# Kernel optimization log

Measured on AMD Instinct MI355X. Metric: run time of the kernel, lower is better.

The kernel has to match this reference:

```python
import jax, jax.numpy as jnp
import numpy as np

N = 50000        # nodes
E = 1_600_000    # edges (avg degree 32)
IN = 8           # in_channels
OUT = 64         # out_channels / hidden
K = 2            # Chebyshev order


def setup_inputs() -> dict:
    key = jax.random.key(0)
    ks = jax.random.split(key, 16)
    w = lambda k, s: (jax.random.normal(k, s, jnp.float32) * 0.05)
    inp = {
        "x": jax.random.normal(ks[0], (N, IN), jnp.float32),
        "H": jax.random.normal(ks[1], (N, OUT), jnp.float32),
        "edge_index": jax.random.randint(ks[2], (2, E), 0, N, dtype=jnp.int64),
    }
    names = [("z_x", IN), ("z_h", OUT), ("r_x", IN), ("r_h", OUT), ("c_x", IN), ("c_h", OUT)]
    for i, (nm, d) in enumerate(names):
        inp["W_" + nm] = w(ks[3 + 2 * i], (K, d, OUT))
        inp["b_" + nm] = w(ks[4 + 2 * i], (OUT,))
    return inp


def _cheb(x, W, b, row, col, norm):
    # PyG-style ChebConv with lambda_max=2: L_hat = -D^{-1/2} A D^{-1/2}
    # Tx0 = x; Tx1 = L_hat x; Tx_k = 2 L_hat Tx_{k-1} - Tx_{k-2}
    out = x @ W[0]
    Tx0 = x
    Tx1 = jax.ops.segment_sum(norm[:, None] * x[col], row, num_segments=N)
    out = out + Tx1 @ W[1]
    for k in range(2, W.shape[0]):
        Tx2 = 2.0 * jax.ops.segment_sum(norm[:, None] * Tx1[col], row, num_segments=N) - Tx0
        out = out + Tx2 @ W[k]
        Tx0, Tx1 = Tx1, Tx2
    return out + b


def reference(x, H, edge_index, W_z_x, b_z_x, W_z_h, b_z_h, W_r_x, b_r_x,
              W_r_h, b_r_h, W_c_x, b_c_x, W_c_h, b_c_h):
    row, col = edge_index[0], edge_index[1]
    deg = jax.ops.segment_sum(jnp.ones((E,), x.dtype), row, num_segments=N)
    dinv = jnp.where(deg > 0, 1.0 / jnp.sqrt(jnp.where(deg > 0, deg, 1.0)), 0.0)
    norm = -dinv[row] * dinv[col]  # sym-normalized, negated adjacency (L - I)

    Z = jax.nn.sigmoid(_cheb(x, W_z_x, b_z_x, row, col, norm)
                       + _cheb(H, W_z_h, b_z_h, row, col, norm))
    R = jax.nn.sigmoid(_cheb(x, W_r_x, b_r_x, row, col, norm)
                       + _cheb(H, W_r_h, b_r_h, row, col, norm))
    C = jnp.tanh(_cheb(x, W_c_x, b_c_x, row, col, norm)
                 + _cheb(R * H, W_c_h, b_c_h, row, col, norm))
    return Z * H + (1.0 - Z) * C
```

## Files before the change

kernel.cpp:

```cpp
#include <hip/hip_runtime.h>
#include <hip/hip_fp16.h>
#include <math.h>

#define IN_CH 8
#define OUT_CH 64
#define NPW 8

__device__ __forceinline__ unsigned short f2h(float f) {
    return __half_as_ushort(__float2half_rn(f));
}
__device__ __forceinline__ float h2f_lo(unsigned v) {
    return __half2float(__ushort_as_half((unsigned short)(v & 0xFFFFu)));
}
__device__ __forceinline__ float h2f_hi(unsigned v) {
    return __half2float(__ushort_as_half((unsigned short)(v >> 16)));
}
__device__ __forceinline__ float sigmoidf(float v) { return 1.0f / (1.0f + expf(-v)); }

__global__ void degP_kernel(const int* __restrict__ row, int* __restrict__ deg,
                            int E, int RPP) {
    int p = blockIdx.x & 7;
    int sub = blockIdx.x >> 3;
    int nsub = gridDim.x >> 3;
    int lo = p * RPP, hi = lo + RPP;
    for (int e = sub * blockDim.x + threadIdx.x; e < E; e += nsub * blockDim.x) {
        int r = row[e];
        if (r >= lo && r < hi) atomicAdd(&deg[r], 1);
    }
}

__global__ void dinv_kernel(const int* __restrict__ deg, float* __restrict__ dinv, int N) {
    int i = blockIdx.x * blockDim.x + threadIdx.x;
    if (i < N) {
        int d = deg[i];
        dinv[i] = (d > 0) ? rsqrtf((float)d) : 0.f;
    }
}

__global__ void scan_kernel(const int* __restrict__ deg, int* __restrict__ rowptr,
                            int* __restrict__ cursor, int N) {
    __shared__ int s_wave[17];
    __shared__ int s_running;
    int tid = threadIdx.x;
    int lane = tid & 63, wid = tid >> 6;
    if (tid == 0) s_running = 0;
    __syncthreads();
    for (int base = 0; base < N; base += 1024) {
        int i = base + tid;
        int v = (i < N) ? deg[i] : 0;
        int incl = v;
#pragma unroll
        for (int off = 1; off < 64; off <<= 1) {
            int t = __shfl_up(incl, off, 64);
            if (lane >= off) incl += t;
        }
        if (lane == 63) s_wave[wid] = incl;
        __syncthreads();
        if (wid == 0) {
            int wv = (lane < 16) ? s_wave[lane] : 0;
            int winc = wv;
#pragma unroll
            for (int off = 1; off < 16; off <<= 1) {
                int t = __shfl_up(winc, off, 64);
                if (lane >= off) winc += t;
            }
            if (lane < 16) s_wave[lane] = winc - wv;
            if (lane == 15) s_wave[16] = winc;
        }
        __syncthreads();
        int run = s_running;
        int excl = run + s_wave[wid] + incl - v;
        if (i < N) { rowptr[i] = excl; cursor[i] = excl; }
        __syncthreads();
        if (tid == 0) s_running = run + s_wave[16];
        __syncthreads();
    }
    if (tid == 0) rowptr[N] = s_running;
}

__global__ void bucketP_kernel(const int* __restrict__ ei, int* __restrict__ cursor,
                               int* __restrict__ col_s, int E, int RPP) {
    int p = blockIdx.x & 7;
    int sub = blockIdx.x >> 3;
    int nsub = gridDim.x >> 3;
    int lo = p * RPP, hi = lo + RPP;
    for (int e = sub * blockDim.x + threadIdx.x; e < E; e += nsub * blockDim.x) {
        int r = ei[e];
        if (r >= lo && r < hi) {
            int c = ei[E + e];
            int pos = atomicAdd(&cursor[r], 1);
            col_s[pos] = c;
        }
    }
}

__global__ void xform_kernel(const float* __restrict__ src, unsigned short* __restrict__ dst,
                             const float* __restrict__ dinv, int total4, int logd) {
    int i = blockIdx.x * blockDim.x + threadIdx.x;
    if (i >= total4) return;
    int el = i * 4;
    float s = dinv[el >> logd];
    float4 v = reinterpret_cast<const float4*>(src)[i];
    ushort4 o;
    o.x = f2h(v.x * s); o.y = f2h(v.y * s); o.z = f2h(v.z * s); o.w = f2h(v.w * s);
    reinterpret_cast<ushort4*>(dst)[i] = o;
}

__global__ void zrow_kernel(unsigned short* xb, unsigned short* Hb, unsigned short* RHb, int N) {
    int t = threadIdx.x;
    if (t < IN_CH) xb[(size_t)N * IN_CH + t] = 0;
    Hb[(size_t)N * OUT_CH + t] = 0;
    RHb[(size_t)N * OUT_CH + t] = 0;
}

__global__ void g64_kernel(const int* __restrict__ rowptr, const int* __restrict__ col_s,
                           const float* __restrict__ dinv, const unsigned short* __restrict__ srcb,
                           float* __restrict__ dst, int N) {
    int n = blockIdx.x * (blockDim.x >> 6) + (threadIdx.x >> 6);
    int lane = threadIdx.x & 63;
    int half = lane >> 5;
    int sl = lane & 31;
    if (n >= N) return;
    int beg = rowptr[n], end = rowptr[n + 1];
    const unsigned* src32 = reinterpret_cast<const unsigned*>(srcb);
    float a0 = 0.f, a1 = 0.f;
    for (int base = beg; base < end; base += 64) {
        int cnt = min(end - base, 64);
        int mycol = col_s[base + min(lane, cnt - 1)];
#pragma unroll 4
        for (int e = 0; e < cnt; e += 2) {
            int idx = e + half;
            int c = __shfl(mycol, idx, 64);
            c = (idx < cnt) ? c : N;
            unsigned v = src32[(c << 5) + sl];
            a0 += h2f_lo(v);
            a1 += h2f_hi(v);
        }
    }
    a0 += __shfl_xor(a0, 32, 64);
    a1 += __shfl_xor(a1, 32, 64);
    if (half == 0) {
        float s = -dinv[n];
        reinterpret_cast<float2*>(dst)[(size_t)n * 32 + sl] = make_float2(s * a0, s * a1);
    }
}

__global__ void g8_kernel(const int* __restrict__ rowptr, const int* __restrict__ col_s,
                          const float* __restrict__ dinv, const unsigned short* __restrict__ srcb,
                          float* __restrict__ dst, int N) {
    int n = blockIdx.x * (blockDim.x >> 6) + (threadIdx.x >> 6);
    int lane = threadIdx.x & 63;
    int g = lane >> 2;
    int o2 = lane & 3;
    if (n >= N) return;
    int beg = rowptr[n], end = rowptr[n + 1];
    const unsigned* src32 = reinterpret_cast<const unsigned*>(srcb);
    float a0 = 0.f, a1 = 0.f;
    for (int j = beg + g; j < end; j += 16) {
        int c = col_s[j];
        unsigned v = src32[(c << 2) + o2];
        a0 += h2f_lo(v);
        a1 += h2f_hi(v);
    }
#pragma unroll
    for (int m = 4; m < 64; m <<= 1) {
        a0 += __shfl_xor(a0, m, 64);
        a1 += __shfl_xor(a1, m, 64);
    }
    if (lane < 4) {
        float s = -dinv[n];
        reinterpret_cast<float2*>(dst)[(size_t)n * 4 + o2] = make_float2(s * a0, s * a1);
    }
}

__global__ __launch_bounds__(256) void gates_kernel(
        const float* __restrict__ x, const float* __restrict__ H,
        const float* __restrict__ Lx, const float* __restrict__ LH,
        const float* __restrict__ dinv,
        const float* __restrict__ Wzx, const float* __restrict__ bzx,
        const float* __restrict__ Wzh, const float* __restrict__ bzh,
        const float* __restrict__ Wrx, const float* __restrict__ brx,
        const float* __restrict__ Wrh, const float* __restrict__ brh,
        float* __restrict__ Z, float* __restrict__ RH, unsigned short* __restrict__ RHb, int N) {
    int wid = threadIdx.x >> 6;
    int lane = threadIdx.x & 63;
    int n0 = blockIdx.x * (4 * NPW) + wid * NPW;

    float axl[NPW], hreg[NPW], lhreg[NPW], accZ[NPW], accR[NPW], dv[NPW];
    float bz = bzx[lane] + bzh[lane];
    float br = brx[lane] + brh[lane];
#pragma unroll
    for (int i = 0; i < NPW; ++i) {
        int nn = min(n0 + i, N - 1);
        axl[i]   = (lane < 8) ? x[(size_t)nn * IN_CH + lane]
                 : (lane < 16 ? Lx[(size_t)nn * IN_CH + (lane - 8)] : 0.f);
        hreg[i]  = H[(size_t)nn * OUT_CH + lane];
        lhreg[i] = LH[(size_t)nn * OUT_CH + lane];
        dv[i]    = dinv[nn];
        accZ[i] = bz;
        accR[i] = br;
    }
#pragma unroll
    for (int k = 0; k < IN_CH; ++k) {
        float wz0 = Wzx[k * 64 + lane], wz1 = Wzx[512 + k * 64 + lane];
        float wr0 = Wrx[k * 64 + lane], wr1 = Wrx[512 + k * 64 + lane];
#pragma unroll
        for (int i = 0; i < NPW; ++i) {
            float xv  = __shfl(axl[i], k, 64);
            float lxv = __shfl(axl[i], k + 8, 64);
            accZ[i] = fmaf(xv, wz0, fmaf(lxv, wz1, accZ[i]));
            accR[i] = fmaf(xv, wr0, fmaf(lxv, wr1, accR[i]));
        }
    }
#pragma unroll 4
    for (int k = 0; k < OUT_CH; ++k) {
        float wh0 = Wzh[k * 64 + lane], wh1 = Wzh[4096 + k * 64 + lane];
        float wr0 = Wrh[k * 64 + lane], wr1 = Wrh[4096 + k * 64 + lane];
#pragma unroll
        for (int i = 0; i < NPW; ++i) {
            float hv  = __shfl(hreg[i], k, 64);
            float lhv = __shfl(lhreg[i], k, 64);
            accZ[i] = fmaf(hv, wh0, fmaf(lhv, wh1, accZ[i]));
            accR[i] = fmaf(hv, wr0, fmaf(lhv, wr1, accR[i]));
        }
    }
#pragma unroll
    for (int i = 0; i < NPW; ++i) {
        int n = n0 + i;
        if (n < N) {
            float z = sigmoidf(accZ[i]);
            float r = sigmoidf(accR[i]);
            float rh = r * hreg[i];
            Z[(size_t)n * OUT_CH + lane]  = z;
            RH[(size_t)n * OUT_CH + lane] = rh;
            RHb[(size_t)n * OUT_CH + lane] = f2h(dv[i] * rh);
        }
    }
}

__global__ __launch_bounds__(256) void final_kernel(
        const float* __restrict__ x, const float* __restrict__ H,
        const float* __restrict__ Lx, const float* __restrict__ RH,
        const float* __restrict__ LRH,
        const float* __restrict__ Wcx, const float* __restrict__ bcx,
        const float* __restrict__ Wch, const float* __restrict__ bch,
        const float* __restrict__ Z, float* __restrict__ out, int N) {
    int wid = threadIdx.x >> 6;
    int lane = threadIdx.x & 63;
    int n0 = blockIdx.x * (4 * NPW) + wid * NPW;

    float axl[NPW], rhreg[NPW], lrhreg[NPW], accC[NPW];
    float bc = bcx[lane] + bch[lane];
#pragma unroll
    for (int i = 0; i < NPW; ++i) {
        int nn = min(n0 + i, N - 1);
        axl[i]    = (lane < 8) ? x[(size_t)nn * IN_CH + lane]
                  : (lane < 16 ? Lx[(size_t)nn * IN_CH + (lane - 8)] : 0.f);
        rhreg[i]  = RH[(size_t)nn * OUT_CH + lane];
        lrhreg[i] = LRH[(size_t)nn * OUT_CH + lane];
        accC[i] = bc;
    }
#pragma unroll
    for (int k = 0; k < IN_CH; ++k) {
        float wc0 = Wcx[k * 64 + lane], wc1 = Wcx[512 + k * 64 + lane];
#pragma unroll
        for (int i = 0; i < NPW; ++i) {
            float xv  = __shfl(axl[i], k, 64);
            float lxv = __shfl(axl[i], k + 8, 64);
            accC[i] = fmaf(xv, wc0, fmaf(lxv, wc1, accC[i]));
        }
    }
#pragma unroll 4
    for (int k = 0; k < OUT_CH; ++k) {
        float wh0 = Wch[k * 64 + lane], wh1 = Wch[4096 + k * 64 + lane];
#pragma unroll
        for (int i = 0; i < NPW; ++i) {
            float rv  = __shfl(rhreg[i], k, 64);
            float lrv = __shfl(lrhreg[i], k, 64);
            accC[i] = fmaf(rv, wh0, fmaf(lrv, wh1, accC[i]));
        }
    }
#pragma unroll
    for (int i = 0; i < NPW; ++i) {
        int n = n0 + i;
        if (n < N) {
            float c = tanhf(accC[i]);
            float z = Z[(size_t)n * OUT_CH + lane];
            float h = H[(size_t)n * OUT_CH + lane];
            out[(size_t)n * OUT_CH + lane] = z * h + (1.0f - z) * c;
        }
    }
}

extern "C" void kernel_launch(void* const* d_in, const int* in_sizes, int n_in,
                              void* d_out, int out_size, void* d_ws, size_t ws_size,
                              hipStream_t stream) {
    const float* x   = (const float*)d_in[0];
    const float* H   = (const float*)d_in[1];
    const int*   ei  = (const int*)d_in[2];
    const float* Wzx = (const float*)d_in[3];
    const float* bzx = (const float*)d_in[4];
    const float* Wzh = (const float*)d_in[5];
    const float* bzh = (const float*)d_in[6];
    const float* Wrx = (const float*)d_in[7];
    const float* brx = (const float*)d_in[8];
    const float* Wrh = (const float*)d_in[9];
    const float* brh = (const float*)d_in[10];
    const float* Wcx = (const float*)d_in[11];
    const float* bcx = (const float*)d_in[12];
    const float* Wch = (const float*)d_in[13];
    const float* bch = (const float*)d_in[14];

    const int N = in_sizes[0] / IN_CH;
    const int E = in_sizes[2] / 2;
    const int RPP = (N + 7) / 8;

    int*   deg    = (int*)d_ws;
    float* dinv   = (float*)(deg + N);
    int*   rowptr = (int*)(dinv + N);
    int*   col_s  = rowptr + (N + 2);
    unsigned short* xb  = (unsigned short*)(col_s + E);
    unsigned short* Hb  = xb + (size_t)(N + 1) * IN_CH;
    unsigned short* RHb = Hb + (size_t)(N + 1) * OUT_CH;
    float* Lx  = (float*)(RHb + (size_t)(N + 1) * OUT_CH);
    float* LH  = Lx + (size_t)N * IN_CH;
    float* Z   = LH + (size_t)N * OUT_CH;
    float* RH  = Z  + (size_t)N * OUT_CH;
    float* LRH = LH;
    int*   cursor = deg;

    hipMemsetAsync(deg, 0, (size_t)N * sizeof(int), stream);

    const int tb = 256;
    const int nblkP = 8 * 128;

    degP_kernel<<<nblkP, tb, 0, stream>>>(ei, deg, E, RPP);
    dinv_kernel<<<(N + tb - 1) / tb, tb, 0, stream>>>(deg, dinv, N);
    scan_kernel<<<1, 1024, 0, stream>>>(deg, rowptr, cursor, N);
    bucketP_kernel<<<nblkP, tb, 0, stream>>>(ei, cursor, col_s, E, RPP);

    {
        int t4 = N * OUT_CH / 4;
        xform_kernel<<<(t4 + tb - 1) / tb, tb, 0, stream>>>(H, Hb, dinv, t4, 6);
        t4 = N * IN_CH / 4;
        xform_kernel<<<(t4 + tb - 1) / tb, tb, 0, stream>>>(x, xb, dinv, t4, 3);
        zrow_kernel<<<1, 64, 0, stream>>>(xb, Hb, RHb, N);
    }

    const int nblk4 = (N + 3) / 4;
    const int nblkD = (N + 4 * NPW - 1) / (4 * NPW);

    g8_kernel <<<nblk4, tb, 0, stream>>>(rowptr, col_s, dinv, xb, Lx, N);
    g64_kernel<<<nblk4, tb, 0, stream>>>(rowptr, col_s, dinv, Hb, LH, N);

    gates_kernel<<<nblkD, tb, 0, stream>>>(x, H, Lx, LH, dinv, Wzx, bzx, Wzh, bzh,
                                           Wrx, brx, Wrh, brh, Z, RH, RHb, N);

    g64_kernel<<<nblk4, tb, 0, stream>>>(rowptr, col_s, dinv, RHb, LRH, N);

    final_kernel<<<nblkD, tb, 0, stream>>>(x, H, Lx, RH, LRH, Wcx, bcx, Wch, bch,
                                           Z, (float*)d_out, N);
}
```

Measured before the change: 612.3 us.

## Fuse neighbor gathers into gate and final GEMM kernels

Removes the separate g8/g64 gather kernels and performs the sparse Laplacian aggregation inside the gates and final kernels. Each wave now gathers its 8 nodes' neighbor sums directly into registers, so the LH/LRH intermediate buffers are no longer written to and re-read from global memory, and two kernel launches go away. The trade-off is that gathers now run in a grid of 32 nodes per block with serialized per-node loops, which may give less memory-level parallelism and load imbalance than the earlier one-node-per-wave launches. There is also more register pressure in the fused kernels.

Measured after the change: 660.9 us. 1.08x slower.

```diff
diff --git a/kernel.cpp b/kernel.cpp
--- a/kernel.cpp
+++ b/kernel.cpp
@@ -113,93 +113,81 @@
     RHb[(size_t)N * OUT_CH + t] = 0;
 }
 
-__global__ void g64_kernel(const int* __restrict__ rowptr, const int* __restrict__ col_s,
-                           const float* __restrict__ dinv, const unsigned short* __restrict__ srcb,
-                           float* __restrict__ dst, int N) {
-    int n = blockIdx.x * (blockDim.x >> 6) + (threadIdx.x >> 6);
-    int lane = threadIdx.x & 63;
-    int half = lane >> 5;
-    int sl = lane & 31;
-    if (n >= N) return;
-    int beg = rowptr[n], end = rowptr[n + 1];
-    const unsigned* src32 = reinterpret_cast<const unsigned*>(srcb);
-    float a0 = 0.f, a1 = 0.f;
-    for (int base = beg; base < end; base += 64) {
-        int cnt = min(end - base, 64);
-        int mycol = col_s[base + min(lane, cnt - 1)];
-#pragma unroll 4
-        for (int e = 0; e < cnt; e += 2) {
-            int idx = e + half;
-            int c = __shfl(mycol, idx, 64);
-            c = (idx < cnt) ? c : N;
-            unsigned v = src32[(c << 5) + sl];
-            a0 += h2f_lo(v);
-            a1 += h2f_hi(v);
-        }
-    }
-    a0 += __shfl_xor(a0, 32, 64);
-    a1 += __shfl_xor(a1, 32, 64);
-    if (half == 0) {
-        float s = -dinv[n];
-        reinterpret_cast<float2*>(dst)[(size_t)n * 32 + sl] = make_float2(s * a0, s * a1);
-    }
-}
-
-__global__ void g8_kernel(const int* __restrict__ rowptr, const int* __restrict__ col_s,
-                          const float* __restrict__ dinv, const unsigned short* __restrict__ srcb,
-                          float* __restrict__ dst, int N) {
-    int n = blockIdx.x * (blockDim.x >> 6) + (threadIdx.x >> 6);
-    int lane = threadIdx.x & 63;
-    int g = lane >> 2;
-    int o2 = lane & 3;
-    if (n >= N) return;
-    int beg = rowptr[n], end = rowptr[n + 1];
-    const unsigned* src32 = reinterpret_cast<const unsigned*>(srcb);
-    float a0 = 0.f, a1 = 0.f;
-    for (int j = beg + g; j < end; j += 16) {
-        int c = col_s[j];
-        unsigned v = src32[(c << 2) + o2];
-        a0 += h2f_lo(v);
-        a1 += h2f_hi(v);
-    }
-#pragma unroll
-    for (int m = 4; m < 64; m <<= 1) {
-        a0 += __shfl_xor(a0, m, 64);
-        a1 += __shfl_xor(a1, m, 64);
-    }
-    if (lane < 4) {
-        float s = -dinv[n];
-        reinterpret_cast<float2*>(dst)[(size_t)n * 4 + o2] = make_float2(s * a0, s * a1);
-    }
-}
-
-__global__ __launch_bounds__(256) void gates_kernel(
+__global__ __launch_bounds__(256) void gatesF_kernel(
         const float* __restrict__ x, const float* __restrict__ H,
-        const float* __restrict__ Lx, const float* __restrict__ LH,
         const float* __restrict__ dinv,
+        const int* __restrict__ rowptr, const int* __restrict__ col_s,
+        const unsigned short* __restrict__ xb, const unsigned short* __restrict__ Hb,
         const float* __restrict__ Wzx, const float* __restrict__ bzx,
         const float* __restrict__ Wzh, const float* __restrict__ bzh,
         const float* __restrict__ Wrx, const float* __restrict__ brx,
         const float* __restrict__ Wrh, const float* __restrict__ brh,
-        float* __restrict__ Z, float* __restrict__ RH, unsigned short* __restrict__ RHb, int N) {
-    int wid = threadIdx.x >> 6;
-    int lane = threadIdx.x & 63;
+        float* __restrict__ Lx, float* __restrict__ Z, float* __restrict__ RH,
+        unsigned short* __restrict__ RHb, int N) {
+    int tid = threadIdx.x;
+    int wid = tid >> 6, lane = tid & 63;
+    int half = lane >> 5, sl = lane & 31;
+    int g4 = lane >> 2, o2 = lane & 3;
     int n0 = blockIdx.x * (4 * NPW) + wid * NPW;
-
-    float axl[NPW], hreg[NPW], lhreg[NPW], accZ[NPW], accR[NPW], dv[NPW];
+    const unsigned* H32 = reinterpret_cast<const unsigned*>(Hb);
+    const unsigned* x32 = reinterpret_cast<const unsigned*>(xb);
+
+    float lhreg[NPW], hreg[NPW], axl[NPW], dv[NPW];
+#pragma unroll
+    for (int i = 0; i < NPW; ++i) {
+        int n = min(n0 + i, N - 1);
+        int beg = rowptr[n], end = rowptr[n + 1];
+        float a0 = 0.f, a1 = 0.f, xa0 = 0.f, xa1 = 0.f;
+        for (int base = beg; base < end; base += 64) {
+            int cnt = min(end - base, 64);
+            int colu = col_s[base + min(lane, cnt - 1)];
+#pragma unroll 4
+            for (int e = 0; e < cnt; e += 2) {
+                int idx = e + half;
+                int c = __shfl(colu, idx, 64);
+                c = (idx < cnt) ? c : N;
+                unsigned v = H32[(c << 5) + sl];
+                a0 += h2f_lo(v);
+                a1 += h2f_hi(v);
+            }
+#pragma unroll
+            for (int e = 0; e < 64; e += 16) {
+                int idx = e + g4;
+                int c = __shfl(colu, idx, 64);
+                c = (idx < cnt) ? c : N;
+                unsigned v = x32[(c << 2) + o2];
+                xa0 += h2f_lo(v);
+                xa1 += h2f_hi(v);
+            }
+        }
+        float s = -dinv[n];
+        dv[i] = dinv[n];
+        a0 += __shfl_xor(a0, 32, 64);
+        a1 += __shfl_xor(a1, 32, 64);
+        float t0 = __shfl(a0, lane >> 1, 64);
+        float t1 = __shfl(a1, lane >> 1, 64);
+        lhreg[i] = ((lane & 1) ? t1 : t0) * s;
+#pragma unroll
+        for (int m = 4; m < 64; m <<= 1) {
+            xa0 += __shfl_xor(xa0, m, 64);
+            xa1 += __shfl_xor(xa1, m, 64);
+        }
+        if (lane < 4 && (n0 + i) < N)
+            reinterpret_cast<float2*>(Lx)[(size_t)(n0 + i) * 4 + o2] =
+                make_float2(s * xa0, s * xa1);
+        int li = (lane >= 8 && lane < 16) ? ((lane - 8) >> 1) : 0;
+        float u0 = __shfl(xa0, li, 64);
+        float u1 = __shfl(xa1, li, 64);
+        axl[i] = (lane < 8) ? x[(size_t)n * IN_CH + lane]
+               : (lane < 16 ? ((lane & 1) ? u1 : u0) * s : 0.f);
+        hreg[i] = H[(size_t)n * OUT_CH + lane];
+    }
+
+    float accZ[NPW], accR[NPW];
     float bz = bzx[lane] + bzh[lane];
     float br = brx[lane] + brh[lane];
 #pragma unroll
-    for (int i = 0; i < NPW; ++i) {
-        int nn = min(n0 + i, N - 1);
-        axl[i]   = (lane < 8) ? x[(size_t)nn * IN_CH + lane]
-                 : (lane < 16 ? Lx[(size_t)nn * IN_CH + (lane - 8)] : 0.f);
-        hreg[i]  = H[(size_t)nn * OUT_CH + lane];
-        lhreg[i] = LH[(size_t)nn * OUT_CH + lane];
-        dv[i]    = dinv[nn];
-        accZ[i] = bz;
-        accR[i] = br;
-    }
+    for (int i = 0; i < NPW; ++i) { accZ[i] = bz; accR[i] = br; }
 #pragma unroll
     for (int k = 0; k < IN_CH; ++k) {
         float wz0 = Wzx[k * 64 + lane], wz1 = Wzx[512 + k * 64 + lane];
@@ -238,28 +226,55 @@
     }
 }
 
-__global__ __launch_bounds__(256) void final_kernel(
+__global__ __launch_bounds__(256) void finalF_kernel(
         const float* __restrict__ x, const float* __restrict__ H,
-        const float* __restrict__ Lx, const float* __restrict__ RH,
-        const float* __restrict__ LRH,
+        const float* __restrict__ dinv,
+        const int* __restrict__ rowptr, const int* __restrict__ col_s,
+        const unsigned short* __restrict__ RHb, const float* __restrict__ Lx,
+        const float* __restrict__ RH,
         const float* __restrict__ Wcx, const float* __restrict__ bcx,
         const float* __restrict__ Wch, const float* __restrict__ bch,
         const float* __restrict__ Z, float* __restrict__ out, int N) {
-    int wid = threadIdx.x >> 6;
-    int lane = threadIdx.x & 63;
+    int tid = threadIdx.x;
+    int wid = tid >> 6, lane = tid & 63;
+    int half = lane >> 5, sl = lane & 31;
     int n0 = blockIdx.x * (4 * NPW) + wid * NPW;
-
-    float axl[NPW], rhreg[NPW], lrhreg[NPW], accC[NPW];
+    const unsigned* R32 = reinterpret_cast<const unsigned*>(RHb);
+
+    float lrhreg[NPW], rhreg[NPW], axl[NPW];
+#pragma unroll
+    for (int i = 0; i < NPW; ++i) {
+        int n = min(n0 + i, N - 1);
+        int beg = rowptr[n], end = rowptr[n + 1];
+        float a0 = 0.f, a1 = 0.f;
+        for (int base = beg; base < end; base += 64) {
+            int cnt = min(end - base, 64);
+            int colu = col_s[base + min(lane, cnt - 1)];
+#pragma unroll 4
+            for (int e = 0; e < cnt; e += 2) {
+                int idx = e + half;
+                int c = __shfl(colu, idx, 64);
+                c = (idx < cnt) ? c : N;
+                unsigned v = R32[(c << 5) + sl];
+                a0 += h2f_lo(v);
+                a1 += h2f_hi(v);
+            }
+        }
+        float s = -dinv[n];
+        a0 += __shfl_xor(a0, 32, 64);
+        a1 += __shfl_xor(a1, 32, 64);
+        float t0 = __shfl(a0, lane >> 1, 64);
+        float t1 = __shfl(a1, lane >> 1, 64);
+        lrhreg[i] = ((lane & 1) ? t1 : t0) * s;
+        rhreg[i]  = RH[(size_t)n * OUT_CH + lane];
+        axl[i] = (lane < 8) ? x[(size_t)n * IN_CH + lane]
+               : (lane < 16 ? Lx[(size_t)n * IN_CH + (lane - 8)] : 0.f);
+    }
+
+    float accC[NPW];
     float bc = bcx[lane] + bch[lane];
 #pragma unroll
-    for (int i = 0; i < NPW; ++i) {
-        int nn = min(n0 + i, N - 1);
-        axl[i]    = (lane < 8) ? x[(size_t)nn * IN_CH + lane]
-                  : (lane < 16 ? Lx[(size_t)nn * IN_CH + (lane - 8)] : 0.f);
-        rhreg[i]  = RH[(size_t)nn * OUT_CH + lane];
-        lrhreg[i] = LRH[(size_t)nn * OUT_CH + lane];
-        accC[i] = bc;
-    }
+    for (int i = 0; i < NPW; ++i) accC[i] = bc;
 #pragma unroll
     for (int k = 0; k < IN_CH; ++k) {
         float wc0 = Wcx[k * 64 + lane], wc1 = Wcx[512 + k * 64 + lane];
@@ -323,10 +338,8 @@
     unsigned short* Hb  = xb + (size_t)(N + 1) * IN_CH;
     unsigned short* RHb = Hb + (size_t)(N + 1) * OUT_CH;
     float* Lx  = (float*)(RHb + (size_t)(N + 1) * OUT_CH);
-    float* LH  = Lx + (size_t)N * IN_CH;
-    float* Z   = LH + (size_t)N * OUT_CH;
+    float* Z   = Lx + (size_t)N * IN_CH;
     float* RH  = Z  + (size_t)N * OUT_CH;
-    float* LRH = LH;
     int*   cursor = deg;
 
     hipMemsetAsync(deg, 0, (size_t)N * sizeof(int), stream);
@@ -347,17 +360,12 @@
         zrow_kernel<<<1, 64, 0, stream>>>(xb, Hb, RHb, N);
     }
 
-    const int nblk4 = (N + 3) / 4;
     const int nblkD = (N + 4 * NPW - 1) / (4 * NPW);
 
-    g8_kernel <<<nblk4, tb, 0, stream>>>(rowptr, col_s, dinv, xb, Lx, N);
-    g64_kernel<<<nblk4, tb, 0, stream>>>(rowptr, col_s, dinv, Hb, LH, N);
-
-    gates_kernel<<<nblkD, tb, 0, stream>>>(x, H, Lx, LH, dinv, Wzx, bzx, Wzh, bzh,
-                                           Wrx, brx, Wrh, brh, Z, RH, RHb, N);
-
-    g64_kernel<<<nblk4, tb, 0, stream>>>(rowptr, col_s, dinv, RHb, LRH, N);
-
-    final_kernel<<<nblkD, tb, 0, stream>>>(x, H, Lx, RH, LRH, Wcx, bcx, Wch, bch,
-                                           Z, (float*)d_out, N);
-}
+    gatesF_kernel<<<nblkD, tb, 0, stream>>>(x, H, dinv, rowptr, col_s, xb, Hb,
+                                            Wzx, bzx, Wzh, bzh, Wrx, brx, Wrh, brh,
+                                            Lx, Z, RH, RHb, N);
+
+    finalF_kernel<<<nblkD, tb, 0, stream>>>(x, H, dinv, rowptr, col_s, RHb, Lx, RH,
+                                            Wcx, bcx, Wch, bch, Z, (float*)d_out, N);
+}
```
